# Performance work log

Measured on AMD Instinct MI355X. Metric: run time of the kernel, lower is better.

Reference implementation:

```python
import jax, jax.numpy as jnp
import numpy as np

EPS = 1e-5

def _layer_norm(x, g, b):
    m = jnp.mean(x, axis=-1, keepdims=True)
    v = jnp.mean((x - m) ** 2, axis=-1, keepdims=True)
    return (x - m) / jnp.sqrt(v + EPS) * g + b

def _dpb(idx, w0, b0, g1, be1, w1, b1, g2, be2, w2, b2, g3, be3, w3, b3):
    # idx: (n, dim, 1) -> (h, n, dim)
    h = idx @ w0 + b0                                   # (n, dim, D)
    h = jax.nn.relu(_layer_norm(h, g1, be1)) @ w1 + b1  # pos1
    h = jax.nn.relu(_layer_norm(h, g2, be2)) @ w2 + b2  # pos2
    h = jax.nn.relu(_layer_norm(h, g3, be3)) @ w3 + b3  # pos3 -> (n, dim, H)
    return jnp.transpose(h, (2, 0, 1))                  # (H, n, dim)

def setup_inputs() -> dict:
    key = jax.random.key(0)
    ks = jax.random.split(key, 6)
    B, H, N, DIM, D = 8, 16, 4096, 64, 64
    s = 0.02
    return {
        "x": jax.random.normal(ks[0], (B, H, N, DIM), jnp.float32),
        "w0": jax.random.normal(ks[1], (1, D), jnp.float32) * s,
        "b0": jnp.zeros((D,), jnp.float32),
        "g1": jnp.ones((D,), jnp.float32),
        "be1": jnp.zeros((D,), jnp.float32),
        "w1": jax.random.normal(ks[2], (D, D), jnp.float32) * s,
        "b1": jnp.zeros((D,), jnp.float32),
        "g2": jnp.ones((D,), jnp.float32),
        "be2": jnp.zeros((D,), jnp.float32),
        "w2": jax.random.normal(ks[3], (D, D), jnp.float32) * s,
        "b2": jnp.zeros((D,), jnp.float32),
        "g3": jnp.ones((D,), jnp.float32),
        "be3": jnp.zeros((D,), jnp.float32),
        "w3": jax.random.normal(ks[4], (D, H), jnp.float32) * s,
        "b3": jnp.zeros((H,), jnp.float32),
    }

def reference(x, w0, b0, g1, be1, w1, b1, g2, be2, w2, b2, g3, be3, w3, b3):
    # DynamicToepliztMultiheadV3 forward (par_type=1, no pad/exp/decay, non-causal)
    n = x.shape[-2]
    dim = x.shape[-1]
    m = n - 1
    dpb_args = (w0, b0, g1, be1, w1, b1, g2, be2, w2, b2, g3, be3, w3, b3)
    scale = 1.0 / (m * dim)
    flat = jnp.arange(1, 1 + m * dim, dtype=x.dtype)
    pos_idx = (flat * scale).reshape(m, dim, 1)
    neg_idx = (-jnp.flip(flat) * scale).reshape(m, dim, 1)  # flip on flat, then reshape (matches torch)
    zero_idx = jnp.zeros((1, dim, 1), x.dtype)
    zero = _dpb(zero_idx, *dpb_args)   # (H, 1, dim)
    pos = _dpb(pos_idx, *dpb_args)     # (H, n-1, dim)
    neg = _dpb(neg_idx, *dpb_args)     # (H, n-1, dim)
    a = jnp.concatenate([zero, pos, zero, neg], axis=1)  # (H, 2n, dim)
    # FFT-based circular (Toeplitz) convolution along seq axis
    y = jnp.fft.rfft(x, 2 * n, axis=-2, norm='ortho')          # (B,H,n+1,dim) complex
    v = jnp.fft.rfft(a, axis=-2)[None]                          # backward norm, as in torch
    out = jnp.fft.irfft(v * y, 2 * n, axis=-2, norm='ortho')[:, :, :n, :]
    return out
```

## Files before the change

### kernel.cpp

```cpp
#include <hip/hip_runtime.h>
#include <math.h>

static const size_t OFF_TW = 0;
static const size_t OFF_V  = 32768;
static const size_t OFF_AT = OFF_V  + (size_t)16 * 64 * 4104 * 8;
static const size_t OFF_ZX = OFF_AT + (size_t)16 * 32 * 8192 * 8;
static const size_t WS_NEED = OFF_ZX + (size_t)128 * 32 * 4096 * 8;

__global__ void __launch_bounds__(256) k_init_tw(float2* __restrict__ tw)
{
    int k = blockIdx.x * 256 + threadIdx.x;
    if (k < 4096) {
        double a = (double)k * (3.14159265358979323846 / 4096.0);
        tw[k] = make_float2((float)cos(a), (float)(-sin(a)));
    }
}

__device__ __forceinline__ void ln_relu_arr(float* b,
                                            const float* __restrict__ g,
                                            const float* __restrict__ be)
{
    float s0 = 0, s1 = 0, s2 = 0, s3 = 0;
    #pragma unroll
    for (int k = 0; k < 64; k += 4) {
        s0 += b[k]; s1 += b[k + 1]; s2 += b[k + 2]; s3 += b[k + 3];
    }
    float m = (s0 + s1 + s2 + s3) * (1.0f / 64.0f);
    float v0 = 0, v1 = 0, v2 = 0, v3 = 0;
    #pragma unroll
    for (int k = 0; k < 64; k += 4) {
        float c0 = b[k] - m, c1 = b[k + 1] - m, c2 = b[k + 2] - m, c3 = b[k + 3] - m;
        v0 = fmaf(c0, c0, v0); v1 = fmaf(c1, c1, v1);
        v2 = fmaf(c2, c2, v2); v3 = fmaf(c3, c3, v3);
    }
    float inv = rsqrtf((v0 + v1 + v2 + v3) * (1.0f / 64.0f) + 1e-5f);
    #pragma unroll
    for (int k = 0; k < 64; ++k)
        b[k] = fmaxf(fmaf((b[k] - m) * inv, g[k], be[k]), 0.0f);
}

__device__ __forceinline__ void matmul64(const float* b, float* o,
                                         const float* __restrict__ w,
                                         const float* __restrict__ bias)
{
    #pragma unroll
    for (int j = 0; j < 64; ++j) o[j] = bias[j];
    #pragma unroll
    for (int k = 0; k < 64; ++k) {
        float bk = b[k];
        const float* wr = w + (k << 6);
        #pragma unroll
        for (int j = 0; j < 64; ++j) o[j] = fmaf(bk, wr[j], o[j]);
    }
}

__global__ void __launch_bounds__(256) k_dpb(
    const float* __restrict__ w0,  const float* __restrict__ b0,
    const float* __restrict__ g1,  const float* __restrict__ be1,
    const float* __restrict__ w1,  const float* __restrict__ b1,
    const float* __restrict__ g2,  const float* __restrict__ be2,
    const float* __restrict__ w2,  const float* __restrict__ b2,
    const float* __restrict__ g3,  const float* __restrict__ be3,
    const float* __restrict__ w3,  const float* __restrict__ b3,
    float* __restrict__ aTf)
{
    int e  = blockIdx.x * 256 + threadIdx.x;
    int r  = e & 8191;
    int dd = e >> 13;
    const float scale = (float)(1.0 / 262080.0);
    float u;
    if (r == 0 || r == 4096) u = 0.0f;
    else if (r < 4096)       u = (float)((r - 1) * 64 + dd + 1) * scale;
    else                     u = -(float)(262080 - ((r - 4097) * 64 + dd)) * scale;

    float b[64], o[64];
    #pragma unroll
    for (int j = 0; j < 64; ++j) b[j] = fmaf(u, w0[j], b0[j]);

    ln_relu_arr(b, g1, be1);
    matmul64(b, o, w1, b1);
    ln_relu_arr(o, g2, be2);
    matmul64(o, b, w2, b2);
    ln_relu_arr(b, g3, be3);

    float f[16];
    #pragma unroll
    for (int j = 0; j < 16; ++j) f[j] = b3[j];
    #pragma unroll
    for (int k = 0; k < 64; ++k) {
        float bk = b[k];
        const float* wr = w3 + (k << 4);
        #pragma unroll
        for (int j = 0; j < 16; ++j) f[j] = fmaf(bk, wr[j], f[j]);
    }
    #pragma unroll
    for (int h = 0; h < 16; ++h) {
        size_t idx = ((size_t)((h << 5) + (dd >> 1)) * 8192 + r) * 2 + (dd & 1);
        aTf[idx] = f[h];
    }
}

__device__ __forceinline__ int sw(int a)
{
    return a ^ ((a >> 4) & 15) ^ ((a >> 8) & 1);
}

__device__ __forceinline__ float2 cmul(float2 a, float2 b)
{
    return make_float2(fmaf(a.x, b.x, -(a.y * b.y)), fmaf(a.x, b.y, a.y * b.x));
}

template<bool INV>
__device__ __forceinline__ float2 twm(float2 a, float wr, float wi)
{
    float i = INV ? -wi : wi;
    return make_float2(fmaf(a.x, wr, -(a.y * i)), fmaf(a.x, i, a.y * wr));
}

template<bool INV>
__device__ __forceinline__ void fft16(float2* z)
{
    const float SQ = 0.70710678118654752440f;
    const float C1 = 0.92387953251128675613f;
    const float S1 = 0.38268343236508977173f;
    #pragma unroll
    for (int b = 0; b < 16; b += 2) {
        float2 u = z[b], t = z[b + 1];
        z[b]     = make_float2(u.x + t.x, u.y + t.y);
        z[b + 1] = make_float2(u.x - t.x, u.y - t.y);
    }
    const float w4r[2] = {1.0f, 0.0f};
    const float w4i[2] = {0.0f, -1.0f};
    #pragma unroll
    for (int b = 0; b < 16; b += 4) {
        #pragma unroll
        for (int j = 0; j < 2; ++j) {
            float2 u = z[b + j];
            float2 t = twm<INV>(z[b + j + 2], w4r[j], w4i[j]);
            z[b + j]     = make_float2(u.x + t.x, u.y + t.y);
            z[b + j + 2] = make_float2(u.x - t.x, u.y - t.y);
        }
    }
    const float w8r[4] = {1.0f, SQ, 0.0f, -SQ};
    const float w8i[4] = {0.0f, -SQ, -1.0f, -SQ};
    #pragma unroll
    for (int b = 0; b < 16; b += 8) {
        #pragma unroll
        for (int j = 0; j < 4; ++j) {
            float2 u = z[b + j];
            float2 t = twm<INV>(z[b + j + 4], w8r[j], w8i[j]);
            z[b + j]     = make_float2(u.x + t.x, u.y + t.y);
            z[b + j + 4] = make_float2(u.x - t.x, u.y - t.y);
        }
    }
    const float wgr[8] = {1.0f, C1, SQ, S1, 0.0f, -S1, -SQ, -C1};
    const float wgi[8] = {0.0f, -S1, -SQ, -C1, -1.0f, -C1, -SQ, -S1};
    #pragma unroll
    for (int j = 0; j < 8; ++j) {
        float2 u = z[j];
        float2 t = twm<INV>(z[j + 8], wgr[j], wgi[j]);
        z[j]     = make_float2(u.x + t.x, u.y + t.y);
        z[j + 8] = make_float2(u.x - t.x, u.y - t.y);
    }
}

template<bool INV>
__device__ __forceinline__ void r16(float2* __restrict__ Z, int base, int j, int L, int s,
                                    const float2* __restrict__ tw)
{
    int addr[16];
    #pragma unroll
    for (int m = 0; m < 16; ++m) addr[m] = sw(base + j + L * m);
    float2 t1 = tw[j * s], t2 = tw[2 * j * s], t4 = tw[4 * j * s], t8 = tw[8 * j * s];
    if (INV) { t1.y = -t1.y; t2.y = -t2.y; t4.y = -t4.y; t8.y = -t8.y; }
    float2 T[16];
    T[1] = t1; T[2] = t2; T[4] = t4; T[8] = t8;
    T[3]  = cmul(t1, t2);   T[5]  = cmul(t1, t4);   T[6]  = cmul(t2, t4);
    T[7]  = cmul(T[3], t4); T[9]  = cmul(t1, t8);   T[10] = cmul(t2, t8);
    T[11] = cmul(T[3], t8); T[12] = cmul(t4, t8);   T[13] = cmul(T[5], t8);
    T[14] = cmul(T[6], t8); T[15] = cmul(T[7], t8);
    const int rv[16] = {0, 8, 4, 12, 2, 10, 6, 14, 1, 9, 5, 13, 3, 11, 7, 15};
    float2 z[16];
    z[0] = Z[addr[0]];
    #pragma unroll
    for (int m = 1; m < 16; ++m) z[m] = cmul(Z[addr[m]], T[rv[m]]);
    fft16<INV>(z);
    #pragma unroll
    for (int q = 0; q < 16; ++q) Z[addr[q]] = z[q];
}

template<int L, bool INV>
__device__ __forceinline__ void reg_stage(float* xr, float* xi,
                                          const float2* __restrict__ tw)
{
    #pragma unroll
    for (int b = 0; b < 32; b += 2 * L) {
        #pragma unroll
        for (int j = 0; j < L; ++j) {
            float2 w = tw[j * (4096 / L)];
            float wr = w.x, wi = INV ? -w.y : w.y;
            int i0 = b + j, i1 = b + j + L;
            float tr = xr[i1] * wr - xi[i1] * wi;
            float ti = xr[i1] * wi + xi[i1] * wr;
            xr[i1] = xr[i0] - tr; xi[i1] = xi[i0] - ti;
            xr[i0] += tr;         xi[i0] += ti;
        }
    }
}

template<bool INV>
__device__ __forceinline__ void fft8192_lds(float2* __restrict__ Z,
                                            const float2* __restrict__ tw)
{
    const int t  = threadIdx.x;
    const int r8 = (int)(__brev((unsigned)t) >> 24);
    float xr[32], xi[32];
    #pragma unroll
    for (int i = 0; i < 32; ++i) {
        int r5 = (int)(__brev((unsigned)i) >> 27);
        float2 v = Z[sw((r5 << 8) | r8)];
        xr[i] = v.x; xi[i] = v.y;
    }
    __syncthreads();
    reg_stage<1,  INV>(xr, xi, tw);
    reg_stage<2,  INV>(xr, xi, tw);
    reg_stage<4,  INV>(xr, xi, tw);
    reg_stage<8,  INV>(xr, xi, tw);
    reg_stage<16, INV>(xr, xi, tw);
    #pragma unroll
    for (int i = 0; i < 32; ++i) Z[sw(32 * t + i)] = make_float2(xr[i], xi[i]);
    __syncthreads();
    {
        int j = t & 31, g = t >> 5;
        r16<INV>(Z, g * 512, j, 32, 16, tw);
        r16<INV>(Z, (g + 8) * 512, j, 32, 16, tw);
    }
    __syncthreads();
    r16<INV>(Z, 0, t, 512, 1, tw);
    r16<INV>(Z, 0, t + 256, 512, 1, tw);
    __syncthreads();
}

__global__ void __launch_bounds__(256, 2) k_vfft(const float2* __restrict__ aT,
                                                 const float2* __restrict__ tw,
                                                 float2* __restrict__ V)
{
    __shared__ float2 Z[8192];
    int blk = blockIdx.x;
    int h = blk >> 5, p = blk & 31;
    const float2* ac = aT + (size_t)(h * 32 + p) * 8192;
    int t = threadIdx.x;
    #pragma unroll
    for (int i = 0; i < 32; ++i) {
        int idx = i * 256 + t;
        Z[sw(idx)] = ac[idx];
    }
    __syncthreads();
    fft8192_lds<false>(Z, tw);
    const float s = 1.0f / 8192.0f;
    float2* V0 = V + (size_t)(h * 64 + 2 * p) * 4104;
    float2* V1 = V0 + 4104;
    for (int k = t; k <= 4096; k += 256) {
        int km = (8192 - k) & 8191;
        float2 z1 = Z[sw(k)], z2 = Z[sw(km)];
        float zr1 = z1.x, zi1 = z1.y;
        float zr2 = z2.x, zi2 = -z2.y;
        float a0r = 0.5f * (zr1 + zr2), a0i = 0.5f * (zi1 + zi2);
        float a1r = 0.5f * (zi1 - zi2), a1i = -0.5f * (zr1 - zr2);
        V0[k] = make_float2(a0r * s, a0i * s);
        V1[k] = make_float2(a1r * s, a1i * s);
    }
}

__global__ void __launch_bounds__(256) k_pack_x(const float* __restrict__ x,
                                                float2* __restrict__ zx)
{
    int blk = blockIdx.x;
    int bh = blk >> 7, rt = blk & 127, r0 = rt << 5;
    __shared__ float tile[64][33];
    const float* xp = x + (size_t)bh * 4096 * 64;
    int tid = threadIdx.x;
    #pragma unroll
    for (int i = 0; i < 8; ++i) {
        int idx = i * 256 + tid;
        int rr = idx >> 6, d = idx & 63;
        tile[d][rr] = xp[(size_t)(r0 + rr) * 64 + d];
    }
    __syncthreads();
    float2* zp = zx + (size_t)bh * 32 * 4096;
    #pragma unroll
    for (int i = 0; i < 4; ++i) {
        int idx = i * 256 + tid;
        int p = idx >> 5, rr = idx & 31;
        zp[(size_t)p * 4096 + r0 + rr] = make_float2(tile[2 * p][rr], tile[2 * p + 1][rr]);
    }
}

__global__ void __launch_bounds__(256, 2) k_conv(float2* __restrict__ zx,
                                                 const float2* __restrict__ V,
                                                 const float2* __restrict__ tw)
{
    __shared__ float2 Z[8192];
    int blk = blockIdx.x;
    int bh = blk >> 5, p = blk & 31, h = bh & 15;
    float2* zc = zx + (size_t)blk * 4096;
    int t = threadIdx.x;
    #pragma unroll
    for (int i = 0; i < 16; ++i) {
        int idx = i * 256 + t;
        Z[sw(idx)] = zc[idx];
        Z[sw(idx + 4096)] = make_float2(0.0f, 0.0f);
    }
    __syncthreads();
    fft8192_lds<false>(Z, tw);
    const float2* V0 = V + (size_t)(h * 64 + 2 * p) * 4104;
    const float2* V1 = V0 + 4104;
    for (int k = t; k <= 4096; k += 256) {
        int km = (8192 - k) & 8191;
        float2 z1 = Z[sw(k)], z2 = Z[sw(km)];
        float zr1 = z1.x, zi1 = z1.y;
        float zr2 = z2.x, zi2 = -z2.y;
        float x0r = 0.5f * (zr1 + zr2), x0i = 0.5f * (zi1 + zi2);
        float x1r = 0.5f * (zi1 - zi2), x1i = -0.5f * (zr1 - zr2);
        float2 v0 = V0[k], v1 = V1[k];
        float y0r = v0.x * x0r - v0.y * x0i, y0i = v0.x * x0i + v0.y * x0r;
        float y1r = v1.x * x1r - v1.y * x1i, y1i = v1.x * x1i + v1.y * x1r;
        Z[sw(k)] = make_float2(y0r - y1i, y0i + y1r);
        if (k > 0 && k < 4096)
            Z[sw(km)] = make_float2(y0r + y1i, y1r - y0i);
    }
    __syncthreads();
    fft8192_lds<true>(Z, tw);
    #pragma unroll
    for (int i = 0; i < 16; ++i) {
        int idx = i * 256 + t;
        zc[idx] = Z[sw(idx)];
    }
}

__global__ void __launch_bounds__(256) k_unpack_out(const float2* __restrict__ zo,
                                                    float* __restrict__ out)
{
    int blk = blockIdx.x;
    int bh = blk >> 7, rt = blk & 127, r0 = rt << 5;
    __shared__ float tile[64][33];
    const float2* zp = zo + (size_t)bh * 32 * 4096;
    int tid = threadIdx.x;
    #pragma unroll
    for (int i = 0; i < 4; ++i) {
        int idx = i * 256 + tid;
        int p = idx >> 5, rr = idx & 31;
        float2 v = zp[(size_t)p * 4096 + r0 + rr];
        tile[2 * p][rr] = v.x; tile[2 * p + 1][rr] = v.y;
    }
    __syncthreads();
    float* op = out + (size_t)bh * 4096 * 64;
    #pragma unroll
    for (int i = 0; i < 8; ++i) {
        int idx = i * 256 + tid;
        int rr = idx >> 6, d = idx & 63;
        op[(size_t)(r0 + rr) * 64 + d] = tile[d][rr];
    }
}

extern "C" void kernel_launch(void* const* d_in, const int* in_sizes, int n_in,
                              void* d_out, int out_size, void* d_ws, size_t ws_size,
                              hipStream_t stream)
{
    (void)in_sizes; (void)n_in; (void)out_size;
    const float* x   = (const float*)d_in[0];
    const float* w0  = (const float*)d_in[1];
    const float* b0  = (const float*)d_in[2];
    const float* g1  = (const float*)d_in[3];
    const float* be1 = (const float*)d_in[4];
    const float* w1  = (const float*)d_in[5];
    const float* b1  = (const float*)d_in[6];
    const float* g2  = (const float*)d_in[7];
    const float* be2 = (const float*)d_in[8];
    const float* w2  = (const float*)d_in[9];
    const float* b2  = (const float*)d_in[10];
    const float* g3  = (const float*)d_in[11];
    const float* be3 = (const float*)d_in[12];
    const float* w3  = (const float*)d_in[13];
    const float* b3  = (const float*)d_in[14];
    float* out = (float*)d_out;
    char* ws = (char*)d_ws;
    if (ws_size < WS_NEED) return;

    float2* tw = (float2*)(ws + OFF_TW);
    float2* V  = (float2*)(ws + OFF_V);
    float2* aT = (float2*)(ws + OFF_AT);
    float2* zx = (float2*)(ws + OFF_ZX);

    k_init_tw<<<16, 256, 0, stream>>>(tw);
    k_dpb<<<2048, 256, 0, stream>>>(w0, b0, g1, be1, w1, b1, g2, be2,
                                    w2, b2, g3, be3, w3, b3, (float*)aT);
    k_vfft<<<512, 256, 0, stream>>>(aT, tw, V);
    k_pack_x<<<16384, 256, 0, stream>>>(x, zx);
    k_conv<<<4096, 256, 0, stream>>>(zx, V, tw);
    k_unpack_out<<<16384, 256, 0, stream>>>((const float2*)zx, out);
}
```

Before: 771.4 us.

## Restructure 8192-point LDS FFT for 512-thread blocks with radix-16 register stages

The in-LDS FFT now uses 512 threads per block. Each thread does a 16-point register FFT instead of 32, followed by two radix-16 LDS passes and a final radix-2 twiddle pass, in place of the earlier 32-point plus two radix-16 layout. The aim is fewer registers per thread and more wavefronts per CU, which should help hide LDS latency in the conv and V-FFT kernels. The cost is an extra synchronised LDS pass and twiddle loads. With 64 KB of LDS per block, occupancy may still be bounded by LDS.

Result: no change. 786.6 us (+2.0%).

```diff
diff --git a/kernel.cpp b/kernel.cpp
--- a/kernel.cpp
+++ b/kernel.cpp
@@ -190,11 +190,11 @@
 }
 
 template<int L, bool INV>
-__device__ __forceinline__ void reg_stage(float* xr, float* xi,
-                                          const float2* __restrict__ tw)
-{
-    #pragma unroll
-    for (int b = 0; b < 32; b += 2 * L) {
+__device__ __forceinline__ void reg_stage16(float* xr, float* xi,
+                                            const float2* __restrict__ tw)
+{
+    #pragma unroll
+    for (int b = 0; b < 16; b += 2 * L) {
         #pragma unroll
         for (int j = 0; j < L; ++j) {
             float2 w = tw[j * (4096 / L)];
@@ -213,35 +213,42 @@
                                             const float2* __restrict__ tw)
 {
     const int t  = threadIdx.x;
-    const int r8 = (int)(__brev((unsigned)t) >> 24);
-    float xr[32], xi[32];
-    #pragma unroll
-    for (int i = 0; i < 32; ++i) {
-        int r5 = (int)(__brev((unsigned)i) >> 27);
-        float2 v = Z[sw((r5 << 8) | r8)];
+    const int r9 = (int)(__brev((unsigned)t) >> 23);
+    float xr[16], xi[16];
+    #pragma unroll
+    for (int i = 0; i < 16; ++i) {
+        int r4 = (int)(__brev((unsigned)i) >> 28);
+        float2 v = Z[sw((r4 << 9) | r9)];
         xr[i] = v.x; xi[i] = v.y;
     }
     __syncthreads();
-    reg_stage<1,  INV>(xr, xi, tw);
-    reg_stage<2,  INV>(xr, xi, tw);
-    reg_stage<4,  INV>(xr, xi, tw);
-    reg_stage<8,  INV>(xr, xi, tw);
-    reg_stage<16, INV>(xr, xi, tw);
-    #pragma unroll
-    for (int i = 0; i < 32; ++i) Z[sw(32 * t + i)] = make_float2(xr[i], xi[i]);
-    __syncthreads();
-    {
-        int j = t & 31, g = t >> 5;
-        r16<INV>(Z, g * 512, j, 32, 16, tw);
-        r16<INV>(Z, (g + 8) * 512, j, 32, 16, tw);
-    }
-    __syncthreads();
-    r16<INV>(Z, 0, t, 512, 1, tw);
-    r16<INV>(Z, 0, t + 256, 512, 1, tw);
-    __syncthreads();
-}
-
-__global__ void __launch_bounds__(256, 2) k_vfft(const float2* __restrict__ aT,
+    reg_stage16<1, INV>(xr, xi, tw);
+    reg_stage16<2, INV>(xr, xi, tw);
+    reg_stage16<4, INV>(xr, xi, tw);
+    reg_stage16<8, INV>(xr, xi, tw);
+    #pragma unroll
+    for (int i = 0; i < 16; ++i) Z[sw(16 * t + i)] = make_float2(xr[i], xi[i]);
+    __syncthreads();
+    r16<INV>(Z, (t >> 4) * 256, t & 15, 16, 32, tw);
+    __syncthreads();
+    r16<INV>(Z, (t >> 8) * 4096, t & 255, 256, 2, tw);
+    __syncthreads();
+    #pragma unroll
+    for (int m = 0; m < 8; ++m) {
+        int k = t + 512 * m;
+        float2 w = tw[k];
+        float wi = INV ? -w.y : w.y;
+        int aL = sw(k), aH = sw(k + 4096);
+        float2 u = Z[aL], v = Z[aH];
+        float tr = fmaf(v.x, w.x, -(v.y * wi));
+        float ti = fmaf(v.x, wi, v.y * w.x);
+        Z[aL] = make_float2(u.x + tr, u.y + ti);
+        Z[aH] = make_float2(u.x - tr, u.y - ti);
+    }
+    __syncthreads();
+}
+
+__global__ void __launch_bounds__(512, 4) k_vfft(const float2* __restrict__ aT,
                                                  const float2* __restrict__ tw,
                                                  float2* __restrict__ V)
 {
@@ -251,8 +258,8 @@
     const float2* ac = aT + (size_t)(h * 32 + p) * 8192;
     int t = threadIdx.x;
     #pragma unroll
-    for (int i = 0; i < 32; ++i) {
-        int idx = i * 256 + t;
+    for (int i = 0; i < 16; ++i) {
+        int idx = i * 512 + t;
         Z[sw(idx)] = ac[idx];
     }
     __syncthreads();
@@ -260,7 +267,7 @@
     const float s = 1.0f / 8192.0f;
     float2* V0 = V + (size_t)(h * 64 + 2 * p) * 4104;
     float2* V1 = V0 + 4104;
-    for (int k = t; k <= 4096; k += 256) {
+    for (int k = t; k <= 4096; k += 512) {
         int km = (8192 - k) & 8191;
         float2 z1 = Z[sw(k)], z2 = Z[sw(km)];
         float zr1 = z1.x, zi1 = z1.y;
@@ -296,7 +303,7 @@
     }
 }
 
-__global__ void __launch_bounds__(256, 2) k_conv(float2* __restrict__ zx,
+__global__ void __launch_bounds__(512, 4) k_conv(float2* __restrict__ zx,
                                                  const float2* __restrict__ V,
                                                  const float2* __restrict__ tw)
 {
@@ -306,8 +313,8 @@
     float2* zc = zx + (size_t)blk * 4096;
     int t = threadIdx.x;
     #pragma unroll
-    for (int i = 0; i < 16; ++i) {
-        int idx = i * 256 + t;
+    for (int i = 0; i < 8; ++i) {
+        int idx = i * 512 + t;
         Z[sw(idx)] = zc[idx];
         Z[sw(idx + 4096)] = make_float2(0.0f, 0.0f);
     }
@@ -315,7 +322,7 @@
     fft8192_lds<false>(Z, tw);
     const float2* V0 = V + (size_t)(h * 64 + 2 * p) * 4104;
     const float2* V1 = V0 + 4104;
-    for (int k = t; k <= 4096; k += 256) {
+    for (int k = t; k <= 4096; k += 512) {
         int km = (8192 - k) & 8191;
         float2 z1 = Z[sw(k)], z2 = Z[sw(km)];
         float zr1 = z1.x, zi1 = z1.y;
@@ -332,8 +339,8 @@
     __syncthreads();
     fft8192_lds<true>(Z, tw);
     #pragma unroll
-    for (int i = 0; i < 16; ++i) {
-        int idx = i * 256 + t;
+    for (int i = 0; i < 8; ++i) {
+        int idx = i * 512 + t;
         zc[idx] = Z[sw(idx)];
     }
 }
@@ -395,8 +402,8 @@
     k_init_tw<<<16, 256, 0, stream>>>(tw);
     k_dpb<<<2048, 256, 0, stream>>>(w0, b0, g1, be1, w1, b1, g2, be2,
                                     w2, b2, g3, be3, w3, b3, (float*)aT);
-    k_vfft<<<512, 256, 0, stream>>>(aT, tw, V);
+    k_vfft<<<512, 512, 0, stream>>>(aT, tw, V);
     k_pack_x<<<16384, 256, 0, stream>>>(x, zx);
-    k_conv<<<4096, 256, 0, stream>>>(zx, V, tw);
+    k_conv<<<4096, 512, 0, stream>>>(zx, V, tw);
     k_unpack_out<<<16384, 256, 0, stream>>>((const float2*)zx, out);
 }
```
